# Performance work log

Hardware: AMD Instinct MI355X
Metric: run time of the kernel (lower is better)

## Reference

```python
import jax, jax.numpy as jnp
import numpy as np

B, C, V, P, E, H, DSC, SD = 4, 1, 64, 4, 64, 8, 256, 1024
NP = (V // P) ** 3  # 4096 patches
SCALE = 1.0 / np.sqrt(E).astype(np.float32)
LN_EPS = 1e-5


def setup_inputs() -> dict:
    key = jax.random.key(0)
    ks = jax.random.split(key, 12)
    w = lambda i, shape, s=0.02: (jax.random.normal(ks[i], shape, jnp.float32) * s)
    return {
        "vox_features": jax.random.normal(ks[0], (B, C, V, V, V), jnp.float32),
        "descriptor": jax.random.normal(ks[1], (B, SD, DSC), jnp.float32),
        "conv_w": w(2, (E, C, P, P, P), 0.1),  # Conv3d weight (OIDHW)
        "conv_b": jnp.zeros((E,), jnp.float32),
        "ln_g": jnp.ones((E,), jnp.float32),
        "ln_b": jnp.zeros((E,), jnp.float32),
        "pos_emb": jnp.zeros((1, NP, E), jnp.float32),
        "wq": w(3, (E, H * E)), "bq": jnp.zeros((H * E,), jnp.float32),
        "wk": w(4, (E, H * E)), "bk": jnp.zeros((H * E,), jnp.float32),
        "wv": w(5, (E, H * E)), "bv": jnp.zeros((H * E,), jnp.float32),
        "wd": w(6, (DSC, E)), "bd": jnp.zeros((E,), jnp.float32),
        "alpha": jnp.float32(1.0),
        "wo": w(7, (H * E, C * P ** 3)), "bo": jnp.zeros((C * P ** 3,), jnp.float32),
    }


def reference(vox_features, descriptor, conv_w, conv_b, ln_g, ln_b, pos_emb,
              wq, bq, wk, bk, wv, bv, wd, bd, alpha, wo, bo):
    # Patch embedding: Conv3d stride=kernel=P -> [B, E, V/P, V/P, V/P]
    emb = jax.lax.conv_general_dilated(
        vox_features, conv_w, window_strides=(P, P, P), padding="VALID",
        dimension_numbers=("NCDHW", "OIDHW", "NCDHW"))
    emb = emb + conv_b[None, :, None, None, None]
    emb = emb.reshape(B, E, -1).transpose(0, 2, 1)  # [B, NP, E]
    # LayerNorm over last dim (torch uses biased variance)
    mu = emb.mean(-1, keepdims=True)
    var = emb.var(-1, keepdims=True)
    emb = (emb - mu) * jax.lax.rsqrt(var + LN_EPS) * ln_g + ln_b
    vox_emb = emb + pos_emb  # [B, NP, E]

    des_emb = descriptor @ wd + bd  # [B, SD, E]

    q = (vox_emb @ wq + bq).reshape(B, NP, H, E).transpose(0, 2, 1, 3)  # [B,H,NP,E]
    k = (des_emb @ wk + bk).reshape(B, SD, H, E).transpose(0, 2, 1, 3)  # [B,H,SD,E]
    v = (des_emb @ wv + bv).reshape(B, SD, H, E).transpose(0, 2, 1, 3)  # [B,H,SD,E]

    # L2 distance: |q|^2 + |k|^2 - 2 q.k
    q2 = jnp.sum(q * q, -1, keepdims=True)                    # [B,H,NP,1]
    k2 = jnp.sum(k * k, -1)[:, :, None, :]                    # [B,H,1,SD]
    dist = q2 + k2 - 2.0 * jnp.einsum("bhqd,bhkd->bhqk", q, k)
    scores = jax.nn.softmax(alpha * jnp.exp(-dist) * SCALE, axis=-1)
    attn = jnp.einsum("bhqk,bhkd->bhqd", scores, v)
    attn = attn.transpose(0, 2, 1, 3).reshape(B, NP, H * E)
    return attn @ wo + bo  # [B, NP, C*P^3]
```

## Files before the change

### kernel.cpp

```cpp
#include <hip/hip_runtime.h>

typedef unsigned short u16;
typedef __bf16 bf16x8 __attribute__((ext_vector_type(8)));
typedef float f32x4 __attribute__((ext_vector_type(4)));

struct alignas(16) V4 { unsigned x, y, z, w; };

#if __has_builtin(__builtin_amdgcn_exp2f)
#define EXP2(x) __builtin_amdgcn_exp2f(x)
#else
#define EXP2(x) __expf((x) * 0.6931471805599453f)
#endif
#define L2E 1.4426950408889634f

__device__ __forceinline__ u16 f2b(float f) {
  unsigned u = __builtin_bit_cast(unsigned, f);
  u += 0x7FFFu + ((u >> 16) & 1u);
  return (u16)(u >> 16);
}
__device__ __forceinline__ unsigned pk2(float a, float b) {
  return (unsigned)f2b(a) | ((unsigned)f2b(b) << 16);
}
__device__ __forceinline__ unsigned pkbf(float a, float b) {
  unsigned d;
  asm("v_cvt_pk_bf16_f32 %0, %1, %2" : "=v"(d) : "v"(a), "v"(b));
  return d;
}
__device__ __forceinline__ bf16x8 asb(V4 v) { return __builtin_bit_cast(bf16x8, v); }
__device__ __forceinline__ bf16x8 mk8(unsigned a, unsigned b, unsigned c, unsigned d) {
  V4 v; v.x = a; v.y = b; v.z = c; v.w = d; return asb(v);
}
__device__ __forceinline__ V4 ldg16(const u16* p) { return *reinterpret_cast<const V4*>(p); }
__device__ __forceinline__ f32x4 mfma16(bf16x8 a, bf16x8 b, f32x4 c) {
  return __builtin_amdgcn_mfma_f32_16x16x32_bf16(a, b, c, 0, 0, 0);
}
__device__ __forceinline__ void gload_lds16(const void* g, void* l) {
  __builtin_amdgcn_global_load_lds(
      (const __attribute__((address_space(1))) int*)g,
      (__attribute__((address_space(3))) int*)l, 16, 0, 0);
}

__global__ __launch_bounds__(256) void k_prep(
    const float* __restrict__ wq, const float* __restrict__ wk,
    const float* __restrict__ wv, const float* __restrict__ wd,
    const float* __restrict__ wo, const float* __restrict__ desc,
    u16* __restrict__ wqT, u16* __restrict__ wkT, u16* __restrict__ wvT,
    u16* __restrict__ wdT, u16* __restrict__ woT, u16* __restrict__ descb) {
  int i = blockIdx.x * 256 + threadIdx.x;
  if (i < 32768) {
    int n = i >> 6, d = i & 63;
    wqT[i] = f2b(wq[d * 512 + n]);
  } else if (i < 65536) {
    int j = i - 32768; int n = j >> 6, d = j & 63;
    wkT[j] = f2b(wk[d * 512 + n]);
  } else if (i < 98304) {
    int j = i - 65536; int n = j >> 6, d = j & 63;
    wvT[j] = f2b(wv[d * 512 + n]);
  } else if (i < 114688) {
    int j = i - 98304; int e = j >> 8, v = j & 255;
    wdT[j] = f2b(wd[v * 64 + e]);
  } else if (i < 147456) {
    int j = i - 114688; int n = j >> 9, kk = j & 511;
    woT[j] = f2b(wo[kk * 64 + n]);
  } else if (i < 409600) {
    int j = (i - 147456) * 4;
    const f32x4 dv = *reinterpret_cast<const f32x4*>(desc + j);
    uint2 pw; pw.x = pk2(dv[0], dv[1]); pw.y = pk2(dv[2], dv[3]);
    *reinterpret_cast<uint2*>(descb + j) = pw;
  }
}

__global__ __launch_bounds__(256) void k_convln(
    const float* __restrict__ vox, const float* __restrict__ cw,
    const float* __restrict__ cb, const float* __restrict__ lng,
    const float* __restrict__ lnb, const float* __restrict__ pos,
    u16* __restrict__ vox_emb) {
  __shared__ float wT[64 * 65];
  __shared__ float pl[4][64];
  const int t = threadIdx.x;
  for (int i = t; i < 4096; i += 256) wT[(i & 63) * 65 + (i >> 6)] = cw[i];
  const int w = t >> 6, lane = t & 63;
  const float cbl = cb[lane], lg = lng[lane], lb = lnb[lane];
  const int i3 = lane >> 4, j3 = (lane >> 2) & 3, k3 = lane & 3;
  for (int i = 0; i < 8; ++i) {
    const int row = blockIdx.x * 32 + w * 8 + i;
    const int b = row >> 12, np = row & 4095;
    const int pd = np >> 8, ph = (np >> 4) & 15, pw = np & 15;
    __syncthreads();
    pl[w][lane] = vox[(size_t)b * 262144 + (size_t)(pd * 4 + i3) * 4096 +
                      (ph * 4 + j3) * 64 + (pw * 4 + k3)];
    __syncthreads();
    float acc = cbl;
    #pragma unroll
    for (int v = 0; v < 64; ++v) acc += pl[w][v] * wT[v * 65 + lane];
    float s1 = acc, s2 = acc * acc;
    #pragma unroll
    for (int m = 1; m < 64; m <<= 1) { s1 += __shfl_xor(s1, m); s2 += __shfl_xor(s2, m); }
    const float mu = s1 * (1.0f / 64.0f);
    const float var = s2 * (1.0f / 64.0f) - mu * mu;
    const float y = (acc - mu) * rsqrtf(var + 1e-5f) * lg + lb + pos[np * 64 + lane];
    vox_emb[(size_t)row * 64 + lane] = f2b(y);
  }
}

__global__ __launch_bounds__(64) void k_des(
    const u16* __restrict__ descb, const u16* __restrict__ wdT,
    const float* __restrict__ bd, u16* __restrict__ desemb) {
  const int lane = threadIdx.x, lr = lane & 15, lc = lane >> 4;
  const int sd0 = blockIdx.x * 16;
  bf16x8 db[8];
  #pragma unroll
  for (int kc = 0; kc < 8; ++kc)
    db[kc] = asb(ldg16(descb + (size_t)(sd0 + lr) * 256 + kc * 32 + lc * 8));
  #pragma unroll
  for (int et = 0; et < 4; ++et) {
    f32x4 acc = {0.f, 0.f, 0.f, 0.f};
    #pragma unroll
    for (int kc = 0; kc < 8; ++kc) {
      const bf16x8 wa = asb(ldg16(wdT + (size_t)(et * 16 + lr) * 256 + kc * 32 + lc * 8));
      acc = mfma16(wa, db[kc], acc);
    }
    const f32x4 bdv = *reinterpret_cast<const f32x4*>(bd + et * 16 + lc * 4);
    uint2 pw;
    pw.x = pk2(acc[0] + bdv[0], acc[1] + bdv[1]);
    pw.y = pk2(acc[2] + bdv[2], acc[3] + bdv[3]);
    *reinterpret_cast<uint2*>(desemb + (size_t)(sd0 + lr) * 64 + et * 16 + lc * 4) = pw;
  }
}

__global__ __launch_bounds__(64) void k_kvproj(
    const u16* __restrict__ desemb, const u16* __restrict__ wkT,
    const float* __restrict__ bk, const u16* __restrict__ wvT,
    const float* __restrict__ bv, u16* __restrict__ kb,
    float* __restrict__ ekl, u16* __restrict__ vtb) {
  const int lane = threadIdx.x, lr = lane & 15, lc = lane >> 4;
  const int x = blockIdx.x, half = blockIdx.y;
  const int b = x >> 6, sb = x & 63, sd0 = sb * 16;
  char* kbc = reinterpret_cast<char*>(kb);
  char* vtc = reinterpret_cast<char*>(vtb);
  const u16* drow = desemb + (size_t)(x * 16 + lr) * 64;
  const bf16x8 da0 = asb(ldg16(drow + lc * 8));
  const bf16x8 da1 = asb(ldg16(drow + 32 + lc * 8));
  const int sd = sd0 + lr, ktK = sd >> 7, rK = sd & 127, xrK = rK & 7;
  float sq = 0.f;
  #pragma unroll
  for (int et = 0; et < 16; ++et) {
    const int etg = half * 16 + et;
    const u16* wrow = wkT + (size_t)(etg * 16 + lr) * 64;
    f32x4 acc = {0.f, 0.f, 0.f, 0.f};
    acc = mfma16(asb(ldg16(wrow + lc * 8)), da0, acc);
    acc = mfma16(asb(ldg16(wrow + 32 + lc * 8)), da1, acc);
    const f32x4 bkv = *reinterpret_cast<const f32x4*>(bk + etg * 16 + lc * 4);
    const float k0 = acc[0] + bkv[0], k1 = acc[1] + bkv[1];
    const float k2 = acc[2] + bkv[2], k3 = acc[3] + bkv[3];
    sq += k0 * k0 + k1 * k1 + k2 * k2 + k3 * k3;
    const int h = etg >> 2, ein = etg & 3;
    const int col16s = (((ein >> 1) * 4 + lc) ^ xrK);
    uint2 pw; pw.x = pk2(k0, k1); pw.y = pk2(k2, k3);
    *reinterpret_cast<uint2*>(kbc + (size_t)(b * 8 + h) * 131072 + ktK * 16384 +
                              rK * 128 + col16s * 16 + (ein & 1) * 8) = pw;
    if ((etg & 3) == 3) {
      float s = sq;
      s += __shfl_xor(s, 16); s += __shfl_xor(s, 32);
      if (lc == 0) ekl[(size_t)(b * 8 + h) * 1024 + sd0 + lr] = -0.5f * s;
      sq = 0.f;
    }
  }
  const int ktV = sb >> 3, kkl = (sb >> 1) & 3, half8 = sb & 1;
  #pragma unroll
  for (int et = 0; et < 16; ++et) {
    const int etg = half * 16 + et;
    const u16* wrow = wvT + (size_t)(etg * 16 + lr) * 64;
    f32x4 acc = {0.f, 0.f, 0.f, 0.f};
    acc = mfma16(da0, asb(ldg16(wrow + lc * 8)), acc);
    acc = mfma16(da1, asb(ldg16(wrow + 32 + lc * 8)), acc);
    const float bvs = bv[etg * 16 + lr];
    const int h = etg >> 2;
    const int e = (etg & 3) * 16 + lr;
    const int col16s = ((kkl * 4 + lc) ^ (e & 7));
    uint2 pw;
    pw.x = pk2(acc[0] + bvs, acc[1] + bvs);
    pw.y = pk2(acc[2] + bvs, acc[3] + bvs);
    *reinterpret_cast<uint2*>(vtc + (size_t)(b * 8 + h) * 131072 + ktV * 16384 +
                              e * 256 + col16s * 16 + half8 * 8) = pw;
  }
}

__global__ __launch_bounds__(256, 4) void k_attn(
    const u16* __restrict__ vox_emb, const u16* __restrict__ wqT,
    const float* __restrict__ bq, const float* __restrict__ alpha,
    const u16* __restrict__ kb, const float* __restrict__ eklg,
    const u16* __restrict__ vtb, u16* __restrict__ attn) {
  __shared__ __align__(16) char Kl[16384];
  __shared__ __align__(16) char Vl[16384];
  const int t = threadIdx.x, w = t >> 6, lane = t & 63, lr = lane & 15, lc = lane >> 4;
  const int bh = blockIdx.y, b = bh >> 3, h = bh & 7;
  const int q0 = blockIdx.x * 128 + w * 32;

  bf16x8 qf0[2], qf1[2];
  float avL[2];
  {
    bf16x8 vb0[2], vb1[2];
    #pragma unroll
    for (int g = 0; g < 2; ++g) {
      const u16* vrow = vox_emb + (size_t)(b * 4096 + q0 + g * 16 + lr) * 64;
      vb0[g] = asb(ldg16(vrow + lc * 8));
      vb1[g] = asb(ldg16(vrow + 32 + lc * 8));
    }
    float sq[2] = {0.f, 0.f};
    unsigned qd[2][4][2];
    #pragma unroll
    for (int et = 0; et < 4; ++et) {
      const u16* wrow = wqT + (size_t)((h * 4 + et) * 16 + lr) * 64;
      const bf16x8 wa0 = asb(ldg16(wrow + lc * 8));
      const bf16x8 wa1 = asb(ldg16(wrow + 32 + lc * 8));
      const f32x4 bqv = *reinterpret_cast<const f32x4*>(bq + (h * 4 + et) * 16 + lc * 4);
      #pragma unroll
      for (int g = 0; g < 2; ++g) {
        f32x4 acc = {0.f, 0.f, 0.f, 0.f};
        acc = mfma16(wa0, vb0[g], acc);
        acc = mfma16(wa1, vb1[g], acc);
        const float v0 = acc[0] + bqv[0], v1 = acc[1] + bqv[1];
        const float v2 = acc[2] + bqv[2], v3 = acc[3] + bqv[3];
        sq[g] += v0 * v0 + v1 * v1 + v2 * v2 + v3 * v3;
        qd[g][et][0] = pk2(v0, v1);
        qd[g][et][1] = pk2(v2, v3);
      }
    }
    const float ca = L2E * 0.125f * alpha[0];
    #pragma unroll
    for (int g = 0; g < 2; ++g) {
      float s = sq[g];
      s += __shfl_xor(s, 16); s += __shfl_xor(s, 32);
      avL[g] = ca * __expf(-s);
      qf0[g] = mk8(qd[g][0][0], qd[g][0][1], qd[g][1][0], qd[g][1][1]);
      qf1[g] = mk8(qd[g][2][0], qd[g][2][1], qd[g][3][0], qd[g][3][1]);
    }
  }

  const f32x4 z = {0.f, 0.f, 0.f, 0.f};
  f32x4 o[2][4];
  float dn[2] = {0.f, 0.f};
  #pragma unroll
  for (int g = 0; g < 2; ++g)
    #pragma unroll
    for (int m = 0; m < 4; ++m) o[g][m] = z;

  const char* kimg = reinterpret_cast<const char*>(kb) + (size_t)bh * 131072;
  const char* vimg = reinterpret_cast<const char*>(vtb) + (size_t)bh * 131072;
  const float* ekh = eklg + (size_t)bh * 1024;
  const int xr = lr & 7;
  const float C2 = 2.8853900817779268f;

  for (int kt = 0; kt < 8; ++kt) {
    {
      const char* kg = kimg + kt * 16384 + w * 4096 + lane * 16;
      const char* vg = vimg + kt * 16384 + w * 4096 + lane * 16;
      char* kl = Kl + w * 4096;
      char* vl = Vl + w * 4096;
      gload_lds16(kg,        kl);
      gload_lds16(kg + 1024, kl + 1024);
      gload_lds16(kg + 2048, kl + 2048);
      gload_lds16(kg + 3072, kl + 3072);
      gload_lds16(vg,        vl);
      gload_lds16(vg + 1024, vl + 1024);
      gload_lds16(vg + 2048, vl + 2048);
      gload_lds16(vg + 3072, vl + 3072);
    }
    __syncthreads();
    #pragma unroll
    for (int c2 = 0; c2 < 4; ++c2) {
      const int kk = kt * 4 + c2;
      const char* kr0 = Kl + (c2 * 32 + lr) * 128;
      const char* kr1 = kr0 + 16 * 128;
      const bf16x8 ka00 = asb(*reinterpret_cast<const V4*>(kr0 + ((lc ^ xr) << 4)));
      const bf16x8 ka01 = asb(*reinterpret_cast<const V4*>(kr0 + (((lc + 4) ^ xr) << 4)));
      const bf16x8 ka10 = asb(*reinterpret_cast<const V4*>(kr1 + ((lc ^ xr) << 4)));
      const bf16x8 ka11 = asb(*reinterpret_cast<const V4*>(kr1 + (((lc + 4) ^ xr) << 4)));
      const int vcol = ((c2 * 4 + lc) ^ xr) << 4;
      const char* vrb = Vl + lr * 256 + vcol;
      const bf16x8 va0 = asb(*reinterpret_cast<const V4*>(vrb));
      const bf16x8 va1 = asb(*reinterpret_cast<const V4*>(vrb + 16 * 256));
      const bf16x8 va2 = asb(*reinterpret_cast<const V4*>(vrb + 32 * 256));
      const bf16x8 va3 = asb(*reinterpret_cast<const V4*>(vrb + 48 * 256));
      const f32x4 ce0 = *reinterpret_cast<const f32x4*>(ekh + kk * 32 + lc * 4);
      const f32x4 ce1 = *reinterpret_cast<const f32x4*>(ekh + kk * 32 + 16 + lc * 4);
      #pragma unroll
      for (int g = 0; g < 2; ++g) {
        f32x4 s0 = ce0, s1 = ce1;
        s0 = mfma16(ka00, qf0[g], s0); s0 = mfma16(ka01, qf1[g], s0);
        s1 = mfma16(ka10, qf0[g], s1); s1 = mfma16(ka11, qf1[g], s1);
        const float t00 = EXP2(C2 * s0[0]), t01 = EXP2(C2 * s0[1]);
        const float t02 = EXP2(C2 * s0[2]), t03 = EXP2(C2 * s0[3]);
        const float t10 = EXP2(C2 * s1[0]), t11 = EXP2(C2 * s1[1]);
        const float t12 = EXP2(C2 * s1[2]), t13 = EXP2(C2 * s1[3]);
        const float p00 = EXP2(avL[g] * t00), p01 = EXP2(avL[g] * t01);
        const float p02 = EXP2(avL[g] * t02), p03 = EXP2(avL[g] * t03);
        const float p10 = EXP2(avL[g] * t10), p11 = EXP2(avL[g] * t11);
        const float p12 = EXP2(avL[g] * t12), p13 = EXP2(avL[g] * t13);
        dn[g] += ((p00 + p01) + (p02 + p03)) + ((p10 + p11) + (p12 + p13));
        const bf16x8 pf = mk8(pkbf(p00, p01), pkbf(p02, p03),
                              pkbf(p10, p11), pkbf(p12, p13));
        o[g][0] = mfma16(va0, pf, o[g][0]);
        o[g][1] = mfma16(va1, pf, o[g][1]);
        o[g][2] = mfma16(va2, pf, o[g][2]);
        o[g][3] = mfma16(va3, pf, o[g][3]);
      }
    }
    __syncthreads();
  }

  u16* obase = attn + (size_t)(b * 4096 + q0 + lr) * 512 + h * 64 + lc * 4;
  #pragma unroll
  for (int g = 0; g < 2; ++g) {
    float s = dn[g];
    s += __shfl_xor(s, 16); s += __shfl_xor(s, 32);
    const float inv = 1.0f / s;
    #pragma unroll
    for (int m = 0; m < 4; ++m) {
      uint2 pw;
      pw.x = pk2(o[g][m][0] * inv, o[g][m][1] * inv);
      pw.y = pk2(o[g][m][2] * inv, o[g][m][3] * inv);
      *reinterpret_cast<uint2*>(obase + (size_t)g * 16 * 512 + m * 16) = pw;
    }
  }
}

__global__ __launch_bounds__(64) void k_out(
    const u16* __restrict__ attn, const u16* __restrict__ woT,
    const float* __restrict__ bo, float* __restrict__ out) {
  const int lane = threadIdx.x, lr = lane & 15, lc = lane >> 4;
  const int np0 = blockIdx.x * 16;
  const u16* arow = attn + (size_t)(np0 + lr) * 512;
  f32x4 acc[4] = {{0.f,0.f,0.f,0.f},{0.f,0.f,0.f,0.f},{0.f,0.f,0.f,0.f},{0.f,0.f,0.f,0.f}};
  #pragma unroll
  for (int kc = 0; kc < 16; ++kc) {
    const bf16x8 bfr = asb(ldg16(arow + kc * 32 + lc * 8));
    #pragma unroll
    for (int et = 0; et < 4; ++et) {
      const bf16x8 wa = asb(ldg16(woT + (size_t)(et * 16 + lr) * 512 + kc * 32 + lc * 8));
      acc[et] = mfma16(wa, bfr, acc[et]);
    }
  }
  #pragma unroll
  for (int et = 0; et < 4; ++et) {
    const f32x4 bov = *reinterpret_cast<const f32x4*>(bo + et * 16 + lc * 4);
    const f32x4 r = acc[et] + bov;
    *reinterpret_cast<f32x4*>(out + (size_t)(np0 + lr) * 64 + et * 16 + lc * 4) = r;
  }
}

extern "C" void kernel_launch(void* const* d_in, const int* in_sizes, int n_in,
                              void* d_out, int out_size, void* d_ws, size_t ws_size,
                              hipStream_t stream) {
  (void)in_sizes; (void)n_in; (void)out_size; (void)ws_size;
  const float* vox   = (const float*)d_in[0];
  const float* desc  = (const float*)d_in[1];
  const float* cw    = (const float*)d_in[2];
  const float* cb    = (const float*)d_in[3];
  const float* lng   = (const float*)d_in[4];
  const float* lnb   = (const float*)d_in[5];
  const float* pos   = (const float*)d_in[6];
  const float* wq    = (const float*)d_in[7];
  const float* bq    = (const float*)d_in[8];
  const float* wk    = (const float*)d_in[9];
  const float* bk    = (const float*)d_in[10];
  const float* wv    = (const float*)d_in[11];
  const float* bv    = (const float*)d_in[12];
  const float* wd    = (const float*)d_in[13];
  const float* bd    = (const float*)d_in[14];
  const float* alpha = (const float*)d_in[15];
  const float* wo    = (const float*)d_in[16];
  const float* bo    = (const float*)d_in[17];
  float* out = (float*)d_out;

  char* ws = (char*)d_ws;
  size_t off = 0;
  auto alloc = [&](size_t bytes) {
    char* p = ws + off;
    off += (bytes + 255) & ~(size_t)255;
    return p;
  };
  u16*   vox_emb = (u16*)alloc((size_t)16384 * 64 * 2);
  u16*   descb   = (u16*)alloc((size_t)4096 * 256 * 2);
  u16*   desemb  = (u16*)alloc((size_t)4096 * 64 * 2);
  u16*   kb      = (u16*)alloc((size_t)4096 * 512 * 2);
  u16*   vtb     = (u16*)alloc((size_t)4096 * 512 * 2);
  float* ekl     = (float*)alloc((size_t)32768 * 4);
  u16*   attn    = (u16*)alloc((size_t)16384 * 512 * 2);
  u16*   wqT     = (u16*)alloc((size_t)32768 * 2);
  u16*   wkT     = (u16*)alloc((size_t)32768 * 2);
  u16*   wvT     = (u16*)alloc((size_t)32768 * 2);
  u16*   wdT     = (u16*)alloc((size_t)16384 * 2);
  u16*   woT     = (u16*)alloc((size_t)32768 * 2);

  k_prep<<<1600, 256, 0, stream>>>(wq, wk, wv, wd, wo, desc, wqT, wkT, wvT, wdT, woT, descb);
  k_convln<<<512, 256, 0, stream>>>(vox, cw, cb, lng, lnb, pos, vox_emb);
  k_des<<<256, 64, 0, stream>>>(descb, wdT, bd, desemb);
  k_kvproj<<<dim3(256, 2), 64, 0, stream>>>(desemb, wkT, bk, wvT, bv, kb, ekl, vtb);
  k_attn<<<dim3(32, 32), 256, 0, stream>>>(vox_emb, wqT, bq, alpha, kb, ekl, vtb, attn);
  k_out<<<1024, 64, 0, stream>>>(attn, woT, bo, out);
}
```

Baseline: 116.6 us.

## Double-buffer K/V tiles in attention, split des/kv-proj grids, drop conv syncs

The attention kernel now stages 64-key K/V tiles plus the key-norm terms into two LDS buffers, loading the next tile while computing on the current one, so global-to-LDS latency overlaps with MFMA work. The K and V global layouts are re-tiled to 64-row chunks to match. k_des and k_kvproj are spread over more blocks (one per output tile or head) to raise parallelism. The per-row barriers in conv+LN are replaced by a single barrier after the weight load, which is safe because each wave only reads its own pl row. Together these change several kernels at once and introduce a layout dependency between the kv-projection and attention kernels.

```diff
diff --git a/kernel.cpp b/kernel.cpp
--- a/kernel.cpp
+++ b/kernel.cpp
@@ -79,6 +79,7 @@
   __shared__ float pl[4][64];
   const int t = threadIdx.x;
   for (int i = t; i < 4096; i += 256) wT[(i & 63) * 65 + (i >> 6)] = cw[i];
+  __syncthreads();
   const int w = t >> 6, lane = t & 63;
   const float cbl = cb[lane], lg = lng[lane], lb = lnb[lane];
   const int i3 = lane >> 4, j3 = (lane >> 2) & 3, k3 = lane & 3;
@@ -86,10 +87,8 @@
     const int row = blockIdx.x * 32 + w * 8 + i;
     const int b = row >> 12, np = row & 4095;
     const int pd = np >> 8, ph = (np >> 4) & 15, pw = np & 15;
-    __syncthreads();
     pl[w][lane] = vox[(size_t)b * 262144 + (size_t)(pd * 4 + i3) * 4096 +
                       (ph * 4 + j3) * 64 + (pw * 4 + k3)];
-    __syncthreads();
     float acc = cbl;
     #pragma unroll
     for (int v = 0; v < 64; ++v) acc += pl[w][v] * wT[v * 65 + lane];
@@ -107,25 +106,19 @@
     const u16* __restrict__ descb, const u16* __restrict__ wdT,
     const float* __restrict__ bd, u16* __restrict__ desemb) {
   const int lane = threadIdx.x, lr = lane & 15, lc = lane >> 4;
-  const int sd0 = blockIdx.x * 16;
-  bf16x8 db[8];
-  #pragma unroll
-  for (int kc = 0; kc < 8; ++kc)
-    db[kc] = asb(ldg16(descb + (size_t)(sd0 + lr) * 256 + kc * 32 + lc * 8));
-  #pragma unroll
-  for (int et = 0; et < 4; ++et) {
-    f32x4 acc = {0.f, 0.f, 0.f, 0.f};
-    #pragma unroll
-    for (int kc = 0; kc < 8; ++kc) {
-      const bf16x8 wa = asb(ldg16(wdT + (size_t)(et * 16 + lr) * 256 + kc * 32 + lc * 8));
-      acc = mfma16(wa, db[kc], acc);
-    }
-    const f32x4 bdv = *reinterpret_cast<const f32x4*>(bd + et * 16 + lc * 4);
-    uint2 pw;
-    pw.x = pk2(acc[0] + bdv[0], acc[1] + bdv[1]);
-    pw.y = pk2(acc[2] + bdv[2], acc[3] + bdv[3]);
-    *reinterpret_cast<uint2*>(desemb + (size_t)(sd0 + lr) * 64 + et * 16 + lc * 4) = pw;
-  }
+  const int sd0 = blockIdx.x * 16, et = blockIdx.y;
+  f32x4 acc = {0.f, 0.f, 0.f, 0.f};
+  #pragma unroll
+  for (int kc = 0; kc < 8; ++kc) {
+    const bf16x8 db = asb(ldg16(descb + (size_t)(sd0 + lr) * 256 + kc * 32 + lc * 8));
+    const bf16x8 wa = asb(ldg16(wdT + (size_t)(et * 16 + lr) * 256 + kc * 32 + lc * 8));
+    acc = mfma16(wa, db, acc);
+  }
+  const f32x4 bdv = *reinterpret_cast<const f32x4*>(bd + et * 16 + lc * 4);
+  uint2 pw;
+  pw.x = pk2(acc[0] + bdv[0], acc[1] + bdv[1]);
+  pw.y = pk2(acc[2] + bdv[2], acc[3] + bdv[3]);
+  *reinterpret_cast<uint2*>(desemb + (size_t)(sd0 + lr) * 64 + et * 16 + lc * 4) = pw;
 }
 
 __global__ __launch_bounds__(64) void k_kvproj(
@@ -134,18 +127,18 @@
     const float* __restrict__ bv, u16* __restrict__ kb,
     float* __restrict__ ekl, u16* __restrict__ vtb) {
   const int lane = threadIdx.x, lr = lane & 15, lc = lane >> 4;
-  const int x = blockIdx.x, half = blockIdx.y;
+  const int x = blockIdx.x, h = blockIdx.y;
   const int b = x >> 6, sb = x & 63, sd0 = sb * 16;
   char* kbc = reinterpret_cast<char*>(kb);
   char* vtc = reinterpret_cast<char*>(vtb);
   const u16* drow = desemb + (size_t)(x * 16 + lr) * 64;
   const bf16x8 da0 = asb(ldg16(drow + lc * 8));
   const bf16x8 da1 = asb(ldg16(drow + 32 + lc * 8));
-  const int sd = sd0 + lr, ktK = sd >> 7, rK = sd & 127, xrK = rK & 7;
+  const int sd = sd0 + lr, ktK = sd >> 6, rK = sd & 63, xrK = sd & 7;
   float sq = 0.f;
   #pragma unroll
-  for (int et = 0; et < 16; ++et) {
-    const int etg = half * 16 + et;
+  for (int et = 0; et < 4; ++et) {
+    const int etg = h * 4 + et;
     const u16* wrow = wkT + (size_t)(etg * 16 + lr) * 64;
     f32x4 acc = {0.f, 0.f, 0.f, 0.f};
     acc = mfma16(asb(ldg16(wrow + lc * 8)), da0, acc);
@@ -154,35 +147,32 @@
     const float k0 = acc[0] + bkv[0], k1 = acc[1] + bkv[1];
     const float k2 = acc[2] + bkv[2], k3 = acc[3] + bkv[3];
     sq += k0 * k0 + k1 * k1 + k2 * k2 + k3 * k3;
-    const int h = etg >> 2, ein = etg & 3;
-    const int col16s = (((ein >> 1) * 4 + lc) ^ xrK);
+    const int col16s = (((et >> 1) * 4 + lc) ^ xrK);
     uint2 pw; pw.x = pk2(k0, k1); pw.y = pk2(k2, k3);
-    *reinterpret_cast<uint2*>(kbc + (size_t)(b * 8 + h) * 131072 + ktK * 16384 +
-                              rK * 128 + col16s * 16 + (ein & 1) * 8) = pw;
-    if ((etg & 3) == 3) {
-      float s = sq;
-      s += __shfl_xor(s, 16); s += __shfl_xor(s, 32);
-      if (lc == 0) ekl[(size_t)(b * 8 + h) * 1024 + sd0 + lr] = -0.5f * s;
-      sq = 0.f;
-    }
-  }
-  const int ktV = sb >> 3, kkl = (sb >> 1) & 3, half8 = sb & 1;
-  #pragma unroll
-  for (int et = 0; et < 16; ++et) {
-    const int etg = half * 16 + et;
+    *reinterpret_cast<uint2*>(kbc + (size_t)(b * 8 + h) * 131072 + ktK * 8192 +
+                              rK * 128 + col16s * 16 + (et & 1) * 8) = pw;
+  }
+  {
+    float s = sq;
+    s += __shfl_xor(s, 16); s += __shfl_xor(s, 32);
+    if (lc == 0) ekl[(size_t)(b * 8 + h) * 1024 + sd0 + lr] = -0.5f * s;
+  }
+  const int ktV = sb >> 2, kkl2 = (sb >> 1) & 1, half8 = sb & 1;
+  #pragma unroll
+  for (int et = 0; et < 4; ++et) {
+    const int etg = h * 4 + et;
     const u16* wrow = wvT + (size_t)(etg * 16 + lr) * 64;
     f32x4 acc = {0.f, 0.f, 0.f, 0.f};
     acc = mfma16(da0, asb(ldg16(wrow + lc * 8)), acc);
     acc = mfma16(da1, asb(ldg16(wrow + 32 + lc * 8)), acc);
     const float bvs = bv[etg * 16 + lr];
-    const int h = etg >> 2;
-    const int e = (etg & 3) * 16 + lr;
-    const int col16s = ((kkl * 4 + lc) ^ (e & 7));
+    const int e = et * 16 + lr;
+    const int col16s = ((kkl2 * 4 + lc) ^ (e & 7));
     uint2 pw;
     pw.x = pk2(acc[0] + bvs, acc[1] + bvs);
     pw.y = pk2(acc[2] + bvs, acc[3] + bvs);
-    *reinterpret_cast<uint2*>(vtc + (size_t)(b * 8 + h) * 131072 + ktV * 16384 +
-                              e * 256 + col16s * 16 + half8 * 8) = pw;
+    *reinterpret_cast<uint2*>(vtc + (size_t)(b * 8 + h) * 131072 + ktV * 8192 +
+                              e * 128 + col16s * 16 + half8 * 8) = pw;
   }
 }
 
@@ -191,8 +181,9 @@
     const float* __restrict__ bq, const float* __restrict__ alpha,
     const u16* __restrict__ kb, const float* __restrict__ eklg,
     const u16* __restrict__ vtb, u16* __restrict__ attn) {
-  __shared__ __align__(16) char Kl[16384];
-  __shared__ __align__(16) char Vl[16384];
+  __shared__ __align__(16) char Kb[2][8192];
+  __shared__ __align__(16) char Vb[2][8192];
+  __shared__ __align__(16) float El[2][64];
   const int t = threadIdx.x, w = t >> 6, lane = t & 63, lr = lane & 15, lc = lane >> 4;
   const int bh = blockIdx.y, b = bh >> 3, h = bh & 7;
   const int q0 = blockIdx.x * 128 + w * 32;
@@ -252,39 +243,34 @@
   const int xr = lr & 7;
   const float C2 = 2.8853900817779268f;
 
-  for (int kt = 0; kt < 8; ++kt) {
-    {
-      const char* kg = kimg + kt * 16384 + w * 4096 + lane * 16;
-      const char* vg = vimg + kt * 16384 + w * 4096 + lane * 16;
-      char* kl = Kl + w * 4096;
-      char* vl = Vl + w * 4096;
-      gload_lds16(kg,        kl);
-      gload_lds16(kg + 1024, kl + 1024);
-      gload_lds16(kg + 2048, kl + 2048);
-      gload_lds16(kg + 3072, kl + 3072);
-      gload_lds16(vg,        vl);
-      gload_lds16(vg + 1024, vl + 1024);
-      gload_lds16(vg + 2048, vl + 2048);
-      gload_lds16(vg + 3072, vl + 3072);
-    }
-    __syncthreads();
-    #pragma unroll
-    for (int c2 = 0; c2 < 4; ++c2) {
-      const int kk = kt * 4 + c2;
-      const char* kr0 = Kl + (c2 * 32 + lr) * 128;
-      const char* kr1 = kr0 + 16 * 128;
+  auto stage = [&](int tt, int pb) {
+    const char* kg = kimg + (size_t)tt * 8192 + w * 2048 + lane * 16;
+    const char* vg = vimg + (size_t)tt * 8192 + w * 2048 + lane * 16;
+    char* kl = Kb[pb] + w * 2048;
+    char* vl = Vb[pb] + w * 2048;
+    gload_lds16(kg, kl); gload_lds16(kg + 1024, kl + 1024);
+    gload_lds16(vg, vl); gload_lds16(vg + 1024, vl + 1024);
+    if (w == 0 && lane < 16)
+      gload_lds16(reinterpret_cast<const char*>(ekh + tt * 64) + lane * 16,
+                  reinterpret_cast<char*>(El[pb]));
+  };
+  auto compute = [&](const char* Kt, const char* Vt, const float* Et) {
+    #pragma unroll
+    for (int c2 = 0; c2 < 2; ++c2) {
+      const char* kr0 = Kt + (c2 * 32 + lr) * 128;
+      const char* kr1 = kr0 + 2048;
       const bf16x8 ka00 = asb(*reinterpret_cast<const V4*>(kr0 + ((lc ^ xr) << 4)));
       const bf16x8 ka01 = asb(*reinterpret_cast<const V4*>(kr0 + (((lc + 4) ^ xr) << 4)));
       const bf16x8 ka10 = asb(*reinterpret_cast<const V4*>(kr1 + ((lc ^ xr) << 4)));
       const bf16x8 ka11 = asb(*reinterpret_cast<const V4*>(kr1 + (((lc + 4) ^ xr) << 4)));
       const int vcol = ((c2 * 4 + lc) ^ xr) << 4;
-      const char* vrb = Vl + lr * 256 + vcol;
+      const char* vrb = Vt + lr * 128 + vcol;
       const bf16x8 va0 = asb(*reinterpret_cast<const V4*>(vrb));
-      const bf16x8 va1 = asb(*reinterpret_cast<const V4*>(vrb + 16 * 256));
-      const bf16x8 va2 = asb(*reinterpret_cast<const V4*>(vrb + 32 * 256));
-      const bf16x8 va3 = asb(*reinterpret_cast<const V4*>(vrb + 48 * 256));
-      const f32x4 ce0 = *reinterpret_cast<const f32x4*>(ekh + kk * 32 + lc * 4);
-      const f32x4 ce1 = *reinterpret_cast<const f32x4*>(ekh + kk * 32 + 16 + lc * 4);
+      const bf16x8 va1 = asb(*reinterpret_cast<const V4*>(vrb + 2048));
+      const bf16x8 va2 = asb(*reinterpret_cast<const V4*>(vrb + 4096));
+      const bf16x8 va3 = asb(*reinterpret_cast<const V4*>(vrb + 6144));
+      const f32x4 ce0 = *reinterpret_cast<const f32x4*>(Et + c2 * 32 + lc * 4);
+      const f32x4 ce1 = *reinterpret_cast<const f32x4*>(Et + c2 * 32 + 16 + lc * 4);
       #pragma unroll
       for (int g = 0; g < 2; ++g) {
         f32x4 s0 = ce0, s1 = ce1;
@@ -307,6 +293,18 @@
         o[g][3] = mfma16(va3, pf, o[g][3]);
       }
     }
+  };
+
+  stage(0, 0);
+  __syncthreads();
+  for (int tt = 0; tt < 8; ++tt) {
+    stage(tt * 2 + 1, 1);
+    __builtin_amdgcn_sched_barrier(0);
+    compute(Kb[0], Vb[0], El[0]);
+    __syncthreads();
+    if (tt < 7) stage(tt * 2 + 2, 0);
+    __builtin_amdgcn_sched_barrier(0);
+    compute(Kb[1], Vb[1], El[1]);
     __syncthreads();
   }
 
@@ -396,8 +394,8 @@
 
   k_prep<<<1600, 256, 0, stream>>>(wq, wk, wv, wd, wo, desc, wqT, wkT, wvT, wdT, woT, descb);
   k_convln<<<512, 256, 0, stream>>>(vox, cw, cb, lng, lnb, pos, vox_emb);
-  k_des<<<256, 64, 0, stream>>>(descb, wdT, bd, desemb);
-  k_kvproj<<<dim3(256, 2), 64, 0, stream>>>(desemb, wkT, bk, wvT, bv, kb, ekl, vtb);
+  k_des<<<dim3(256, 4), 64, 0, stream>>>(descb, wdT, bd, desemb);
+  k_kvproj<<<dim3(256, 8), 64, 0, stream>>>(desemb, wkT, bk, wvT, bv, kb, ekl, vtb);
   k_attn<<<dim3(32, 32), 256, 0, stream>>>(vox_emb, wqT, bq, alpha, kb, ekl, vtb, attn);
   k_out<<<1024, 64, 0, stream>>>(attn, woT, bo, out);
 }
```

Result: slower. 127.4 us (+9.3%).
